# Kernel tuning notes

Measured on AMD Instinct MI355X. Metric: run time of the kernel, lower is better.

Reference implementation:

```python
import jax, jax.numpy as jnp
import numpy as np

B, N, FIN, H, D = 4, 2048, 128, 4, 64
ALPHA = 0.2  # LeakyReLU negative slope


def _xavier_uniform(key, shape):
    fan_in, fan_out = shape[0], shape[1]
    limit = float(np.sqrt(6.0 / (fan_in + fan_out)))
    return jax.random.uniform(key, shape, jnp.float32, -limit, limit)


def setup_inputs() -> dict:
    key = jax.random.key(0)
    k1, k2, k3, k4 = jax.random.split(key, 4)
    x = jax.random.normal(k1, (B, N, FIN), jnp.float32)
    adj = jax.random.randint(k2, (B, N, N), 0, 2, jnp.int32)  # dense 0/1 mask
    W = _xavier_uniform(k3, (FIN, H * D))
    a = _xavier_uniform(k4, (2 * D, 1))
    return {"x": x, "adj": adj, "W": W, "a": a}


def reference(x, adj, W, a):
    Bb, Nn, _ = x.shape
    Dd = a.shape[0] // 2
    Hh = W.shape[1] // Dd
    # h: [B, N, H, D]
    h = (x @ W).reshape(Bb, Nn, Hh, Dd)
    # Additive attention: e[b,i,j,h] = leakyrelu(a1 . h[b,i,h] + a2 . h[b,j,h])
    a1 = a[:Dd, 0]
    a2 = a[Dd:, 0]
    ei = jnp.einsum('bnhd,d->bnh', h, a1)  # source (row i) term
    ej = jnp.einsum('bnhd,d->bnh', h, a2)  # dest (col j) term
    e = ei[:, :, None, :] + ej[:, None, :, :]  # [B, N, N, H]
    e = jnp.where(e >= 0, e, ALPHA * e)  # LeakyReLU
    e = jnp.where(adj[..., None] == 0, -jnp.inf, e)
    att = jax.nn.softmax(e, axis=2)  # softmax over neighbors j
    # dropout is a no-op in eval mode (training=False)
    out = jnp.einsum('bijh,bjhd->bihd', att, h)  # [B, N, H, D]
    return out.mean(axis=2)  # mean over heads -> [B, N, D]
```

## Files before the change

### kernel.cpp

```cpp
#include <hip/hip_runtime.h>

#define NN 2048
#define NH 4
#define DD 64
#define FIN 128
#define NB 4
#define LOG2E 1.44269504f

typedef unsigned short u16;
typedef unsigned int u32;
typedef short sh8 __attribute__((ext_vector_type(8)));
typedef float f32x4 __attribute__((ext_vector_type(4)));

static __device__ __forceinline__ u16 f2bf(float f) {
    u32 u = __builtin_bit_cast(u32, f);
    u += 0x7fffu + ((u >> 16) & 1u);
    return (u16)(u >> 16);
}
static __device__ __forceinline__ u32 pk_bf(float a, float b) {
    u32 ua = __builtin_bit_cast(u32, a) + 0x8000u;
    u32 ub = __builtin_bit_cast(u32, b) + 0x8000u;
    return __builtin_amdgcn_perm(ub, ua, 0x07060302u);
}
static __device__ __forceinline__ u32 cvt_pk(float a, float b) {
    u32 r;
    asm("v_cvt_pk_bf16_f32 %0, %1, %2" : "=v"(r) : "v"(a), "v"(b));
    return r;
}
static __device__ __forceinline__ float fast_exp2(float x) {
    float r;
    asm("v_exp_f32 %0, %1" : "=v"(r) : "v"(x));
    return r;
}

static __device__ __forceinline__ void cd_probe(int ln15, int q, int* irow, int* icol) {
    sh8 pa, pb, qa, qb;
    #pragma unroll
    for (int ii = 0; ii < 8; ++ii) {
        pa[ii] = (short)f2bf((float)ln15);
        pb[ii] = 0;
        qa[ii] = 0;
        qb[ii] = (short)f2bf((float)ln15);
    }
    if (q == 0) { pb[0] = (short)f2bf(1.0f); qa[0] = (short)f2bf(1.0f); }
    f32x4 z = {};
    f32x4 prow = __builtin_amdgcn_mfma_f32_16x16x32_bf16(pa, pb, z, 0, 0, 0);
    f32x4 pcol = __builtin_amdgcn_mfma_f32_16x16x32_bf16(qa, qb, z, 0, 0, 0);
    #pragma unroll
    for (int r = 0; r < 4; ++r) {
        irow[r] = (int)(prow[r] + 0.5f);
        icol[r] = (int)(pcol[r] + 0.5f);
    }
}


__global__ __launch_bounds__(256)
void k_prep(const float* __restrict__ W, u16* __restrict__ WT) {
    const int bt  = blockIdx.x;
    const int kt  = bt & 3;
    const int ct8 = bt >> 2;
    __shared__ float tile[32][33];
    const int tid = threadIdx.x;
    const int rr = tid >> 5, cc = tid & 31;
    #pragma unroll
    for (int i = 0; i < 4; ++i)
        tile[rr + 8 * i][cc] = W[(size_t)(kt * 32 + rr + 8 * i) * 256 + ct8 * 32 + cc];
    __syncthreads();
    #pragma unroll
    for (int i = 0; i < 4; ++i)
        WT[(size_t)(ct8 * 32 + rr + 8 * i) * FIN + kt * 32 + cc] = f2bf(tile[cc][rr + 8 * i]);
}

__global__ __launch_bounds__(256)
void k_gemm_h(const float* __restrict__ x, const u16* __restrict__ WT,
              const float* __restrict__ a,
              u16* __restrict__ hTf, float* __restrict__ Ea_g, float* __restrict__ Ga_g,
              float* __restrict__ Fb_g, float* __restrict__ Hb_g) {
    const int nb = blockIdx.x, b = blockIdx.y;
    const int tid = threadIdx.x, hd = tid >> 6, lane = tid & 63, ln15 = lane & 15, q = lane >> 4;
    const int q8 = q * 8;
    const int n0 = nb * 64;

    __shared__ u16 xs[64][136];
    __shared__ float cs[NH][4][16][20];
    {
        const int col = (tid & 31) * 4;
        const int r0  = tid >> 5;
        #pragma unroll
        for (int rr = 0; rr < 8; ++rr) {
            const int row = r0 + rr * 8;
            const float4 v = *(const float4*)(x + ((size_t)(b * NN + n0 + row)) * FIN + col);
            *(u32*)&xs[row][col]     = pk_bf(v.x, v.y);
            *(u32*)&xs[row][col + 2] = pk_bf(v.z, v.w);
        }
    }
    __syncthreads();

    int irow[4], icol[4];
    cd_probe(ln15, q, irow, icol);

    f32x4 acc[4][4] = {};
    #pragma unroll
    for (int ks = 0; ks < 4; ++ks) {
        sh8 af[4], bfr[4];
        #pragma unroll
        for (int ct = 0; ct < 4; ++ct)
            af[ct] = *(const sh8*)(WT + (size_t)(hd * 64 + ct * 16 + ln15) * FIN + ks * 32 + q8);
        #pragma unroll
        for (int nt = 0; nt < 4; ++nt)
            bfr[nt] = *(const sh8*)&xs[nt * 16 + ln15][ks * 32 + q8];
        #pragma unroll
        for (int ct = 0; ct < 4; ++ct)
            #pragma unroll
            for (int nt = 0; nt < 4; ++nt)
                acc[ct][nt] = __builtin_amdgcn_mfma_f32_16x16x32_bf16(af[ct], bfr[nt], acc[ct][nt], 0, 0, 0);
    }

    float eip[4] = {}, ejq[4] = {};
    #pragma unroll
    for (int ct = 0; ct < 4; ++ct) {
        #pragma unroll
        for (int nt = 0; nt < 4; ++nt)
            #pragma unroll
            for (int r = 0; r < 4; ++r)
                cs[hd][nt][irow[r]][icol[r]] = acc[ct][nt][r];

        #pragma unroll
        for (int p = 0; p < 2; ++p) {
            const float4 c0 = *(const float4*)&cs[hd][2 * p + (q >> 1)][ln15][(q & 1) * 8];
            const float4 c1 = *(const float4*)&cs[hd][2 * p + (q >> 1)][ln15][(q & 1) * 8 + 4];
            uint4 o;
            o.x = pk_bf(c0.x, c0.y); o.y = pk_bf(c0.z, c0.w);
            o.z = pk_bf(c1.x, c1.y); o.w = pk_bf(c1.z, c1.w);
            *(uint4*)(hTf + ((((size_t)(b * NH + hd) * 64 + nb * 2 + p) * 4 + ct) * 512) + lane * 8) = o;
        }

        float a1v[4], a2v[4];
        #pragma unroll
        for (int r = 0; r < 4; ++r) {
            const int d = ct * 16 + 4 * q + r;
            a1v[r] = a[d] * LOG2E;
            a2v[r] = a[64 + d] * LOG2E;
        }
        #pragma unroll
        for (int nt = 0; nt < 4; ++nt)
            #pragma unroll
            for (int r = 0; r < 4; ++r) {
                const float v = cs[hd][nt][4 * q + r][ln15];
                eip[nt] += v * a1v[r];
                ejq[nt] += v * a2v[r];
            }
    }
    #pragma unroll
    for (int nt = 0; nt < 4; ++nt) {
        eip[nt] += __shfl_xor(eip[nt], 16);
        eip[nt] += __shfl_xor(eip[nt], 32);
        ejq[nt] += __shfl_xor(ejq[nt], 16);
        ejq[nt] += __shfl_xor(ejq[nt], 32);
    }
    if (lane < 16) {
        const size_t bhd = (size_t)(b * NH + hd) * NN;
        #pragma unroll
        for (int nt = 0; nt < 4; ++nt) {
            const size_t idx = bhd + n0 + nt * 16 + lane;
            Ea_g[idx] = fast_exp2(eip[nt]);
            Ga_g[idx] = fast_exp2(0.2f * eip[nt]);
            Fb_g[idx] = fast_exp2(ejq[nt]);
            Hb_g[idx] = fast_exp2(0.2f * ejq[nt]);
        }
    }
}

template <int NJT>
__global__ __launch_bounds__(256, 3)
void k_attn(const int* __restrict__ adj, const u16* __restrict__ hTf,
            const float* __restrict__ Ea, const float* __restrict__ Ga,
            const float* __restrict__ Fb, const float* __restrict__ Hb,
            float* __restrict__ o_part, float* __restrict__ l_part) {
    const int ib = blockIdx.x, js = blockIdx.y, b = blockIdx.z;
    const int js_n = gridDim.y;
    const int tid = threadIdx.x, hd = tid >> 6, lane = tid & 63, ln15 = lane & 15, q = lane >> 4;
    const int q8 = q * 8;
    const int iA = ib * 32 + ln15;
    const int jt0 = js * NJT;

    __shared__ u32   pmsk[32][NJT * 16 + 4];
    __shared__ float fjs[NH][NJT * 32];
    __shared__ float hjs[NH][NJT * 32];

    {
        const int row = (hd << 3) + (lane >> 3);
        const int lk = lane & 7;
        const int* abase = adj + (size_t)(b * NN + ib * 32 + row) * NN + jt0 * 32 + lk * 4;
        #pragma unroll
        for (int jb = 0; jb < NJT; jb += 8) {
            int4 vv[8];
            #pragma unroll
            for (int u = 0; u < 8; ++u)
                vv[u] = *(const int4*)(abase + (jb + u) * 32);
            #pragma unroll
            for (int u = 0; u < 8; ++u) {
                uint2 wv;
                wv.x = (vv[u].x ? 0xFFFFu : 0u) | (vv[u].y ? 0xFFFF0000u : 0u);
                wv.y = (vv[u].z ? 0xFFFFu : 0u) | (vv[u].w ? 0xFFFF0000u : 0u);
                *(uint2*)&pmsk[row][(jb + u) * 16 + lk * 2] = wv;
            }
        }
    }
    const size_t bhd = (size_t)(b * NH + hd) * NN;
    {
        const float* fsrc = Fb + bhd + jt0 * 32;
        const float* hsrc = Hb + bhd + jt0 * 32;
        #pragma unroll
        for (int u = 0; u < NJT / 8; ++u) {
            const int o4 = (u * 64 + lane) * 4;
            *(float4*)&fjs[hd][o4] = *(const float4*)(fsrc + o4);
            *(float4*)&hjs[hd][o4] = *(const float4*)(hsrc + o4);
        }
    }
    __syncthreads();

    int irow[4], icol[4];
    cd_probe(ln15, q, irow, icol);

    const float EiA = Ea[bhd + iA];
    const float GiA = Ga[bhd + iA];
    const float EiB = Ea[bhd + iA + 16];
    const float GiB = Ga[bhd + iA + 16];
    const u16*  hfp = hTf + (size_t)(b * NH + hd) * (64 * 2048) + (size_t)lane * 8;

    sh8 ones;
    #pragma unroll
    for (int ii = 0; ii < 8; ++ii) ones[ii] = (short)0x3F80;

    f32x4 acc[8] = {};
    f32x4 accl[2] = {};

    sh8 H[2][4];
    #pragma unroll
    for (int s = 0; s < 2; ++s)
        #pragma unroll
        for (int k = 0; k < 4; ++k)
            H[s][k] = *(const sh8*)(hfp + (size_t)(jt0 + s) * 2048 + k * 512);

    #pragma unroll
    for (int t = 0; t < NJT; ++t) {
        const uint4 mwA = *(const uint4*)&pmsk[ln15][t * 16 + q * 4];
        const uint4 mwB = *(const uint4*)&pmsk[ln15 + 16][t * 16 + q * 4];
        const float4 f0 = *(const float4*)&fjs[hd][t * 32 + q8];
        const float4 f1 = *(const float4*)&fjs[hd][t * 32 + q8 + 4];
        const float4 h0 = *(const float4*)&hjs[hd][t * 32 + q8];
        const float4 h1 = *(const float4*)&hjs[hd][t * 32 + q8 + 4];
        const float pf[8] = { f0.x, f0.y, f0.z, f0.w, f1.x, f1.y, f1.z, f1.w };
        const float ph[8] = { h0.x, h0.y, h0.z, h0.w, h1.x, h1.y, h1.z, h1.w };
        const u32 mA[4] = { mwA.x, mwA.y, mwA.z, mwA.w };
        const u32 mB[4] = { mwB.x, mwB.y, mwB.z, mwB.w };

        uint4 uA, uB;
        u32 wA[4], wB[4];
        #pragma unroll
        for (int p = 0; p < 4; ++p) {
            const float a0 = fmaxf(EiA * pf[2 * p], GiA * ph[2 * p]);
            const float a1 = fmaxf(EiA * pf[2 * p + 1], GiA * ph[2 * p + 1]);
            wA[p] = cvt_pk(a0, a1) & mA[p];
            const float b0 = fmaxf(EiB * pf[2 * p], GiB * ph[2 * p]);
            const float b1 = fmaxf(EiB * pf[2 * p + 1], GiB * ph[2 * p + 1]);
            wB[p] = cvt_pk(b0, b1) & mB[p];
        }
        uA.x = wA[0]; uA.y = wA[1]; uA.z = wA[2]; uA.w = wA[3];
        uB.x = wB[0]; uB.y = wB[1]; uB.z = wB[2]; uB.w = wB[3];
        const sh8 av = __builtin_bit_cast(sh8, uA);
        const sh8 bv = __builtin_bit_cast(sh8, uB);

        acc[0] = __builtin_amdgcn_mfma_f32_16x16x32_bf16(av, H[t & 1][0], acc[0], 0, 0, 0);
        acc[1] = __builtin_amdgcn_mfma_f32_16x16x32_bf16(av, H[t & 1][1], acc[1], 0, 0, 0);
        acc[2] = __builtin_amdgcn_mfma_f32_16x16x32_bf16(av, H[t & 1][2], acc[2], 0, 0, 0);
        acc[3] = __builtin_amdgcn_mfma_f32_16x16x32_bf16(av, H[t & 1][3], acc[3], 0, 0, 0);
        accl[0] = __builtin_amdgcn_mfma_f32_16x16x32_bf16(av, ones, accl[0], 0, 0, 0);
        acc[4] = __builtin_amdgcn_mfma_f32_16x16x32_bf16(bv, H[t & 1][0], acc[4], 0, 0, 0);
        acc[5] = __builtin_amdgcn_mfma_f32_16x16x32_bf16(bv, H[t & 1][1], acc[5], 0, 0, 0);
        acc[6] = __builtin_amdgcn_mfma_f32_16x16x32_bf16(bv, H[t & 1][2], acc[6], 0, 0, 0);
        acc[7] = __builtin_amdgcn_mfma_f32_16x16x32_bf16(bv, H[t & 1][3], acc[7], 0, 0, 0);
        accl[1] = __builtin_amdgcn_mfma_f32_16x16x32_bf16(bv, ones, accl[1], 0, 0, 0);

        if (t + 2 < NJT) {
            #pragma unroll
            for (int k = 0; k < 4; ++k)
                H[t & 1][k] = *(const sh8*)(hfp + (size_t)(jt0 + t + 2) * 2048 + k * 512);
        }
    }

    const size_t pbA = (((size_t)b * 128 + ib * 2 + 0) * js_n + js) * NH + hd;
    const size_t pbB = (((size_t)b * 128 + ib * 2 + 1) * js_n + js) * NH + hd;
    #pragma unroll
    for (int r = 0; r < 4; ++r) {
        l_part[pbA * 16 + irow[r]] = accl[0][r];
        l_part[pbB * 16 + irow[r]] = accl[1][r];
    }
    float* opA = o_part + pbA * 1024;
    float* opB = o_part + pbB * 1024;
    #pragma unroll
    for (int dt = 0; dt < 4; ++dt)
        #pragma unroll
        for (int r = 0; r < 4; ++r) {
            opA[(size_t)irow[r] * 64 + dt * 16 + icol[r]] = acc[dt][r];
            opB[(size_t)irow[r] * 64 + dt * 16 + icol[r]] = acc[4 + dt][r];
        }
}

template <int JS>
__global__ __launch_bounds__(256)
void k_combine(const float* __restrict__ o_part, const float* __restrict__ l_part,
               float* __restrict__ out) {
    const int ib = blockIdx.x, b = blockIdx.y;
    const int tid = threadIdx.x;
    const int i = tid >> 4, d4 = (tid & 15) * 4;
    float4 sacc = {0.f, 0.f, 0.f, 0.f};
    #pragma unroll
    for (int h = 0; h < NH; ++h) {
        float l = 0.f;
        float4 oh = {0.f, 0.f, 0.f, 0.f};
        #pragma unroll
        for (int js = 0; js < JS; ++js) {
            const size_t pbase = (((size_t)b * 128 + ib) * JS + js) * NH + h;
            l += l_part[pbase * 16 + i];
            const float4 ov = *(const float4*)(o_part + pbase * 1024 + (size_t)i * 64 + d4);
            oh.x += ov.x; oh.y += ov.y; oh.z += ov.z; oh.w += ov.w;
        }
        const float inv = 0.25f / l;
        sacc.x += oh.x * inv; sacc.y += oh.y * inv;
        sacc.z += oh.z * inv; sacc.w += oh.w * inv;
    }
    *(float4*)(out + ((size_t)(b * NN) + ib * 16 + i) * DD + d4) = sacc;
}

extern "C" void kernel_launch(void* const* d_in, const int* in_sizes, int n_in,
                              void* d_out, int out_size, void* d_ws, size_t ws_size,
                              hipStream_t stream) {
    const float* x = nullptr; const int* adj = nullptr;
    const float* W = nullptr; const float* a = nullptr;
    for (int i = 0; i < n_in; ++i) {
        switch (in_sizes[i]) {
            case NB * NN * FIN:  x   = (const float*)d_in[i]; break;
            case NB * NN * NN:   adj = (const int*)d_in[i];   break;
            case FIN * 256:      W   = (const float*)d_in[i]; break;
            case 2 * DD:         a   = (const float*)d_in[i]; break;
            default: break;
        }
    }
    if (!x)   x   = (const float*)d_in[0];
    if (!adj) adj = (const int*)d_in[1];
    if (!W)   W   = (const float*)d_in[2];
    if (!a)   a   = (const float*)d_in[3];
    float* out = (float*)d_out;

    char* ws = (char*)d_ws;
    u16*   WT  = (u16*)(ws);
    float* Ea  = (float*)(ws + 65536);
    float* Ga  = (float*)(ws + 196608);
    float* Fb  = (float*)(ws + 327680);
    float* Hb  = (float*)(ws + 458752);
    u16*   hTf = (u16*)(ws + 589824);
    float* l_p = (float*)(ws + 4784128);
    float* o_p = (float*)(ws + 5308416);

    const size_t need4 = 5308416 + (size_t)4 * 8388608;
    const int js_n = (ws_size >= need4) ? 4 : 2;

    k_prep<<<dim3(32), dim3(256), 0, stream>>>(W, WT);
    k_gemm_h<<<dim3(32, NB), dim3(256), 0, stream>>>(x, WT, a, hTf, Ea, Ga, Fb, Hb);
    if (js_n == 4)
        k_attn<16><<<dim3(64, 4, NB), dim3(256), 0, stream>>>(adj, hTf, Ea, Ga, Fb, Hb, o_p, l_p);
    else
        k_attn<32><<<dim3(64, 2, NB), dim3(256), 0, stream>>>(adj, hTf, Ea, Ga, Fb, Hb, o_p, l_p);
    if (js_n == 4)      k_combine<4><<<dim3(128, NB), dim3(256), 0, stream>>>(o_p, l_p, out);
    else                k_combine<2><<<dim3(128, NB), dim3(256), 0, stream>>>(o_p, l_p, out);
}
```

Before: 134.6 us.

## Pack adjacency mask into bitfields in LDS and halve the j-split

Stores the adjacency mask as one bit per neighbour (a 32-bit word per row and j-tile, built with lane shuffles) instead of 16-bit expanded masks, which cuts LDS footprint and per-iteration LDS read width. The smaller LDS use lets launch bounds ask for 4 blocks per CU. The j dimension is now split into 2 parts instead of 4, so each block handles longer tiles and the partial buffers and combine work shrink. The price is extra ALU work to expand the bits inside the inner loop, fewer blocks in the grid (512), and higher register pressure under the tighter launch bound.

```diff
diff --git a/kernel.cpp b/kernel.cpp
--- a/kernel.cpp
+++ b/kernel.cpp
@@ -172,7 +172,7 @@
 }
 
 template <int NJT>
-__global__ __launch_bounds__(256, 3)
+__global__ __launch_bounds__(256, 4)
 void k_attn(const int* __restrict__ adj, const u16* __restrict__ hTf,
             const float* __restrict__ Ea, const float* __restrict__ Ga,
             const float* __restrict__ Fb, const float* __restrict__ Hb,
@@ -184,7 +184,7 @@
     const int iA = ib * 32 + ln15;
     const int jt0 = js * NJT;
 
-    __shared__ u32   pmsk[32][NJT * 16 + 4];
+    __shared__ u32   mlds[32][NJT + 1];
     __shared__ float fjs[NH][NJT * 32];
     __shared__ float hjs[NH][NJT * 32];
 
@@ -200,10 +200,13 @@
                 vv[u] = *(const int4*)(abase + (jb + u) * 32);
             #pragma unroll
             for (int u = 0; u < 8; ++u) {
-                uint2 wv;
-                wv.x = (vv[u].x ? 0xFFFFu : 0u) | (vv[u].y ? 0xFFFF0000u : 0u);
-                wv.y = (vv[u].z ? 0xFFFFu : 0u) | (vv[u].w ? 0xFFFF0000u : 0u);
-                *(uint2*)&pmsk[row][(jb + u) * 16 + lk * 2] = wv;
+                u32 nib = (vv[u].x ? 1u : 0u) | (vv[u].y ? 2u : 0u) |
+                          (vv[u].z ? 4u : 0u) | (vv[u].w ? 8u : 0u);
+                u32 w = nib << (4 * lk);
+                w |= __shfl_xor(w, 1);
+                w |= __shfl_xor(w, 2);
+                w |= __shfl_xor(w, 4);
+                if (lk == 0) mlds[row][jb + u] = w;
             }
         }
     }
@@ -245,27 +248,29 @@
 
     #pragma unroll
     for (int t = 0; t < NJT; ++t) {
-        const uint4 mwA = *(const uint4*)&pmsk[ln15][t * 16 + q * 4];
-        const uint4 mwB = *(const uint4*)&pmsk[ln15 + 16][t * 16 + q * 4];
+        const u32 mqA = mlds[ln15][t] >> q8;
+        const u32 mqB = mlds[ln15 + 16][t] >> q8;
         const float4 f0 = *(const float4*)&fjs[hd][t * 32 + q8];
         const float4 f1 = *(const float4*)&fjs[hd][t * 32 + q8 + 4];
         const float4 h0 = *(const float4*)&hjs[hd][t * 32 + q8];
         const float4 h1 = *(const float4*)&hjs[hd][t * 32 + q8 + 4];
         const float pf[8] = { f0.x, f0.y, f0.z, f0.w, f1.x, f1.y, f1.z, f1.w };
         const float ph[8] = { h0.x, h0.y, h0.z, h0.w, h1.x, h1.y, h1.z, h1.w };
-        const u32 mA[4] = { mwA.x, mwA.y, mwA.z, mwA.w };
-        const u32 mB[4] = { mwB.x, mwB.y, mwB.z, mwB.w };
 
         uint4 uA, uB;
         u32 wA[4], wB[4];
         #pragma unroll
         for (int p = 0; p < 4; ++p) {
+            const u32 mA32 = ((0u - ((mqA >> (2 * p)) & 1u)) & 0xFFFFu) |
+                             ((0u - ((mqA >> (2 * p + 1)) & 1u)) << 16);
+            const u32 mB32 = ((0u - ((mqB >> (2 * p)) & 1u)) & 0xFFFFu) |
+                             ((0u - ((mqB >> (2 * p + 1)) & 1u)) << 16);
             const float a0 = fmaxf(EiA * pf[2 * p], GiA * ph[2 * p]);
             const float a1 = fmaxf(EiA * pf[2 * p + 1], GiA * ph[2 * p + 1]);
-            wA[p] = cvt_pk(a0, a1) & mA[p];
+            wA[p] = cvt_pk(a0, a1) & mA32;
             const float b0 = fmaxf(EiB * pf[2 * p], GiB * ph[2 * p]);
             const float b1 = fmaxf(EiB * pf[2 * p + 1], GiB * ph[2 * p + 1]);
-            wB[p] = cvt_pk(b0, b1) & mB[p];
+            wB[p] = cvt_pk(b0, b1) & mB32;
         }
         uA.x = wA[0]; uA.y = wA[1]; uA.z = wA[2]; uA.w = wA[3];
         uB.x = wB[0]; uB.y = wB[1]; uB.z = wB[2]; uB.w = wB[3];
@@ -364,15 +369,15 @@
     float* l_p = (float*)(ws + 4784128);
     float* o_p = (float*)(ws + 5308416);
 
-    const size_t need4 = 5308416 + (size_t)4 * 8388608;
-    const int js_n = (ws_size >= need4) ? 4 : 2;
+    const size_t need2 = 5308416 + (size_t)2 * 8388608;
+    const int js_n = (ws_size >= need2) ? 2 : 1;
 
     k_prep<<<dim3(32), dim3(256), 0, stream>>>(W, WT);
     k_gemm_h<<<dim3(32, NB), dim3(256), 0, stream>>>(x, WT, a, hTf, Ea, Ga, Fb, Hb);
-    if (js_n == 4)
-        k_attn<16><<<dim3(64, 4, NB), dim3(256), 0, stream>>>(adj, hTf, Ea, Ga, Fb, Hb, o_p, l_p);
+    if (js_n == 2)
+        k_attn<32><<<dim3(64, 2, NB), dim3(256), 0, stream>>>(adj, hTf, Ea, Ga, Fb, Hb, o_p, l_p);
     else
-        k_attn<32><<<dim3(64, 2, NB), dim3(256), 0, stream>>>(adj, hTf, Ea, Ga, Fb, Hb, o_p, l_p);
-    if (js_n == 4)      k_combine<4><<<dim3(128, NB), dim3(256), 0, stream>>>(o_p, l_p, out);
-    else                k_combine<2><<<dim3(128, NB), dim3(256), 0, stream>>>(o_p, l_p, out);
-}
+        k_attn<64><<<dim3(64, 1, NB), dim3(256), 0, stream>>>(adj, hTf, Ea, Ga, Fb, Hb, o_p, l_p);
+    if (js_n == 2) k_combine<2><<<dim3(128, NB), dim3(256), 0, stream>>>(o_p, l_p, out);
+    else           k_combine<1><<<dim3(128, NB), dim3(256), 0, stream>>>(o_p, l_p, out);
+}
```

Measured after the change: 132.9 us (median of 2 runs). About the same (-1.2%).
